# Kernel tuning notes

Measured on AMD Instinct MI355X. Metric: run time of the kernel, lower is better.

## Reference

```python
import jax, jax.numpy as jnp
import numpy as np

MARGIN = 1.0

def setup_inputs() -> dict:
    key = jax.random.key(0)
    k1, k2, k3 = jax.random.split(key, 3)
    B, C, D = 65536, 1000, 512
    x = jax.random.normal(k1, (B, D), dtype=jnp.float32)
    x = x / jnp.linalg.norm(x, axis=1, keepdims=True)  # docstring: ||x||2 = 1
    labels = jax.random.randint(k2, (B,), 0, C, dtype=jnp.int64)
    centers = jax.random.normal(k3, (C, D), dtype=jnp.float32)
    return {"x": x, "labels": labels, "centers": centers}

def reference(x, labels, centers):
    # l2Norm applied to the centers (module is only used when l2Norm is truthy)
    c = centers / jnp.linalg.norm(centers, axis=1, keepdims=True)  # (C, D)
    # cosine distance to every center: one batched GEMM instead of per-sample loop
    dist = 1.0 - jnp.einsum("bd,cd->bc", x, c)                      # (B, C)
    pos = jnp.take_along_axis(dist, labels[:, None], axis=1)[:, 0]  # (B,)
    # min over all classes != label: mask own class with +inf
    same = jnp.arange(c.shape[0])[None, :] == labels[:, None]       # (B, C)
    neg = jnp.min(jnp.where(same, jnp.inf, dist), axis=1)           # (B,)
    # sum of per-sample hinge losses divided by batch size == mean
    return jnp.mean(jax.nn.relu(pos + MARGIN - neg))
```

## Files before the change

kernel.cpp:

```cpp
#include <hip/hip_runtime.h>
#include <stdint.h>

typedef short v8s __attribute__((ext_vector_type(8)));
typedef short v4s __attribute__((ext_vector_type(4)));
typedef float v4f __attribute__((ext_vector_type(4)));

#define BM 256
#define BN 128
#define BKH 32
#define TSH ((BM + BN) * BKH)
#define POS_INF __builtin_inff()

typedef __attribute__((address_space(3))) unsigned int lds_uint;
typedef const __attribute__((address_space(1))) unsigned int glb_uint;

__device__ __forceinline__ void load16_lds(const void* g, void* l) {
    __builtin_amdgcn_global_load_lds((glb_uint*)g, (lds_uint*)l, 16, 0, 0);
}

__device__ __forceinline__ short f2bf(float f) {
    uint32_t u = __builtin_bit_cast(uint32_t, f);
    u += 0x7fffu + ((u >> 16) & 1u);
    return (short)(u >> 16);
}

__global__ void prep(const float* __restrict__ centers,
                     unsigned short* __restrict__ cbf,
                     int C, int D, int CP, int CB,
                     const float* __restrict__ x,
                     unsigned short* __restrict__ xbf, size_t nx,
                     int* __restrict__ cnt, int NB,
                     float* __restrict__ out) {
    const int b = blockIdx.x;
    const int t = threadIdx.x;
    if (b == 0 && t == 0) out[0] = 0.0f;
    if (b < CB) {
        const int g = b * 256 + t;
        if (g < NB) cnt[g] = 0;
        const int wave = t >> 6, lane = t & 63;
        const int row = b * 4 + wave;
        if (row >= CP) return;
        if (row >= C) {
            v4s z = {0, 0, 0, 0};
            for (int d = lane * 4; d < D; d += 256)
                *(v4s*)&cbf[(size_t)row * D + d] = z;
            return;
        }
        const float* src = centers + (size_t)row * D;
        float ss = 0.0f;
        for (int d = lane * 4; d < D; d += 256) {
            v4f f = *(const v4f*)&src[d];
            ss += f.x * f.x + f.y * f.y + f.z * f.z + f.w * f.w;
        }
        #pragma unroll
        for (int off = 32; off; off >>= 1) ss += __shfl_xor(ss, off, 64);
        const float rn = rsqrtf(ss);
        for (int d = lane * 4; d < D; d += 256) {
            v4f f = *(const v4f*)&src[d];
            v4s s;
            s.x = f2bf(f.x * rn); s.y = f2bf(f.y * rn);
            s.z = f2bf(f.z * rn); s.w = f2bf(f.w * rn);
            *(v4s*)&cbf[(size_t)row * D + d] = s;
        }
    } else {
        const size_t i = ((size_t)(b - CB) * 256 + t) * 8;
        if (i >= nx) return;
        v4f f0 = *(const v4f*)&x[i];
        v4f f1 = *(const v4f*)&x[i + 4];
        v8s s;
        s[0] = f2bf(f0.x); s[1] = f2bf(f0.y); s[2] = f2bf(f0.z); s[3] = f2bf(f0.w);
        s[4] = f2bf(f1.x); s[5] = f2bf(f1.y); s[6] = f2bf(f1.z); s[7] = f2bf(f1.w);
        *(v8s*)&xbf[i] = s;
    }
}

__global__ void __launch_bounds__(512)
gemm_fused(const unsigned short* __restrict__ xbf,
           const unsigned short* __restrict__ cbf,
           const int* __restrict__ labels,
           float* __restrict__ pos, float* __restrict__ partial,
           int* __restrict__ cnt,
           int Bt, int C, int D, int NT, float margin,
           float* __restrict__ out) {
    __shared__ short LDSbuf[2 * TSH];
    short* As0 = LDSbuf;
    short* Bs0 = LDSbuf + BM * BKH;
    short* As1 = LDSbuf + TSH;
    short* Bs1 = As1 + BM * BKH;

    const int t   = threadIdx.x;
    const int bid = blockIdx.x;
    const int xcd = bid & 7;
    const int per = bid >> 3;
    const int rowblk = (per >> 3) * 8 + xcd;
    const int nt     = per & 7;
    const int row0 = rowblk * BM;
    const int n0   = nt * BN;

    const int lane = t & 63;
    const int wave = t >> 6;
    const int wm = wave >> 1;
    const int wn = wave & 1;
    const int l15 = lane & 15, q = lane >> 4;

    const int rsub = lane >> 2;
    const int csrc = (lane & 3) ^ (rsub & 3);

    int myLab = 0;
    if (t < BM) myLab = labels[row0 + t];

    v4f acc[4][4];
    #pragma unroll
    for (int i = 0; i < 4; ++i)
        #pragma unroll
        for (int j = 0; j < 4; ++j)
            acc[i][j] = (v4f){0.f, 0.f, 0.f, 0.f};

    #define STAGE(As_, Bs_, k0_) do {                                        \
        load16_lds(&xbf[(size_t)(row0 + wave * 32 + rsub) * D + (k0_) + csrc * 8], \
                   &(As_)[(wave * 32) * BKH]);                               \
        load16_lds(&xbf[(size_t)(row0 + wave * 32 + 16 + rsub) * D + (k0_) + csrc * 8], \
                   &(As_)[(wave * 32 + 16) * BKH]);                          \
        load16_lds(&cbf[(size_t)(n0 + wave * 16 + rsub) * D + (k0_) + csrc * 8], \
                   &(Bs_)[(wave * 16) * BKH]);                               \
    } while (0)

    #define TILE(As_, Bs_) do {                                              \
        v8s a[4], b[4];                                                      \
        _Pragma("unroll")                                                    \
        for (int i = 0; i < 4; ++i)                                          \
            a[i] = *(const v8s*)&(As_)[(wm * 64 + i * 16 + l15) * BKH        \
                                       + ((q ^ (l15 & 3)) << 3)];            \
        _Pragma("unroll")                                                    \
        for (int j = 0; j < 4; ++j)                                          \
            b[j] = *(const v8s*)&(Bs_)[(wn * 64 + j * 16 + l15) * BKH        \
                                       + ((q ^ (l15 & 3)) << 3)];            \
        _Pragma("unroll")                                                    \
        for (int i = 0; i < 4; ++i)                                          \
            _Pragma("unroll")                                                \
            for (int j = 0; j < 4; ++j)                                      \
                acc[i][j] = __builtin_amdgcn_mfma_f32_16x16x32_bf16(         \
                    a[i], b[j], acc[i][j], 0, 0, 0);                         \
    } while (0)

    STAGE(As0, Bs0, 0);
    __syncthreads();

    const int KT2 = D / (2 * BKH);
    for (int kt2 = 0; kt2 < KT2; ++kt2) {
        const int k0 = kt2 * 64;
        STAGE(As1, Bs1, k0 + 32);
        TILE(As0, Bs0);
        __syncthreads();
        if (kt2 + 1 < KT2) STAGE(As0, Bs0, k0 + 64);
        TILE(As1, Bs1);
        __syncthreads();
    }

    #undef STAGE
    #undef TILE

    int*   Ls    = (int*)LDSbuf;
    float* sMinW = (float*)((char*)LDSbuf + 1024);
    int*   sLast = (int*)((char*)LDSbuf + 3072);
    float* wsum  = (float*)((char*)LDSbuf + 3088);
    if (t < BM) Ls[t] = myLab;
    __syncthreads();

    #pragma unroll
    for (int i = 0; i < 4; ++i) {
        #pragma unroll
        for (int rg = 0; rg < 4; ++rg) {
            const int row_l = wm * 64 + i * 16 + q * 4 + rg;
            const int lab = Ls[row_l];
            float m = POS_INF;
            #pragma unroll
            for (int j = 0; j < 4; ++j) {
                const int col = n0 + wn * 64 + j * 16 + l15;
                const float d = 1.0f - acc[i][j][rg];
                if (col == lab)
                    __hip_atomic_store(&pos[row0 + row_l], d,
                                       __ATOMIC_RELAXED, __HIP_MEMORY_SCOPE_AGENT);
                else if (col < C) m = fminf(m, d);
            }
            m = fminf(m, __shfl_xor(m, 1, 64));
            m = fminf(m, __shfl_xor(m, 2, 64));
            m = fminf(m, __shfl_xor(m, 4, 64));
            m = fminf(m, __shfl_xor(m, 8, 64));
            if (l15 == 0) sMinW[wn * BM + row_l] = m;
        }
    }
    __syncthreads();
    if (t < BM) {
        const float m = fminf(sMinW[t], sMinW[BM + t]);
        __hip_atomic_store(&partial[(size_t)nt * Bt + row0 + t], m,
                           __ATOMIC_RELAXED, __HIP_MEMORY_SCOPE_AGENT);
    }
    __syncthreads();

    if (t == 0) {
        __builtin_amdgcn_s_waitcnt(0);
        const int old = __hip_atomic_fetch_add(&cnt[rowblk], 1,
                                               __ATOMIC_RELAXED,
                                               __HIP_MEMORY_SCOPE_AGENT);
        *sLast = (old == NT - 1);
    }
    __syncthreads();
    if (!*sLast) return;

    float hng = 0.0f;
    if (t < BM) {
        const int r = row0 + t;
        float neg = POS_INF;
        for (int tt = 0; tt < NT; ++tt)
            neg = fminf(neg, __hip_atomic_load(&partial[(size_t)tt * Bt + r],
                                               __ATOMIC_RELAXED,
                                               __HIP_MEMORY_SCOPE_AGENT));
        const float p = __hip_atomic_load(&pos[r], __ATOMIC_RELAXED,
                                          __HIP_MEMORY_SCOPE_AGENT);
        hng = fmaxf(0.0f, p + margin - neg);
    }
    #pragma unroll
    for (int off = 32; off; off >>= 1) hng += __shfl_down(hng, off, 64);
    if (lane == 0) wsum[wave] = hng;
    __syncthreads();
    if (t == 0) {
        float s = 0.0f;
        #pragma unroll
        for (int w = 0; w < 8; ++w) s += wsum[w];
        atomicAdd(out, s * (1.0f / (float)Bt));
    }
}

extern "C" void kernel_launch(void* const* d_in, const int* in_sizes, int n_in,
                              void* d_out, int out_size, void* d_ws, size_t ws_size,
                              hipStream_t stream) {
    const float* x       = (const float*)d_in[0];
    const int*   labels  = (const int*)d_in[1];
    const float* centers = (const float*)d_in[2];
    float* out = (float*)d_out;

    const int Bt = in_sizes[1];
    const int D  = in_sizes[0] / Bt;
    const int C  = in_sizes[2] / D;
    const int NT = (C + BN - 1) / BN;
    const int CP = NT * BN;
    const int NB = Bt / BM;

    char* ws = (char*)d_ws;
    unsigned short* cbf = (unsigned short*)ws;
    size_t off = (size_t)CP * D * 2;
    off = (off + 255) & ~(size_t)255;
    float* pos = (float*)(ws + off);      off += (size_t)Bt * 4;
    float* partial = (float*)(ws + off);  off += (size_t)NT * Bt * 4;
    int* cnt = (int*)(ws + off);          off += (size_t)NB * 4;
    off = (off + 255) & ~(size_t)255;
    unsigned short* xbf = (unsigned short*)(ws + off);

    const size_t nx = (size_t)Bt * D;
    const int CB = CP / 4;
    const int XB = (int)((nx / 8 + 255) / 256);
    prep<<<CB + XB, 256, 0, stream>>>(centers, cbf, C, D, CP, CB, x, xbf, nx,
                                      cnt, NB, out);

    gemm_fused<<<NB * NT, 512, 0, stream>>>(xbf, cbf, labels, pos, partial, cnt,
                                            Bt, C, D, NT, 1.0f, out);
}
```

Baseline: 291.9 us.

## Triple-buffer LDS tiles with vmcnt waits and change swizzle pattern

Replaces the double-buffered K loop, which had two full __syncthreads per pair of tiles, with a three-stage ring buffer held in dynamic shared memory. Each iteration waits only until the oldest stage's async global-to-LDS loads have landed (vmcnt(3)) and then issues a raw barrier, so two tiles of loads can be in flight while MFMAs run. The XOR swizzle for the LDS layout also changes to use bits 1-2 of the row index, aimed at cutting bank conflicts. LDS use rises to about 72KB per block, which may limit occupancy, and the hand-placed waitcnt relies on exactly three loads per stage.

Result: faster. 285.0 us (-2.3%).

```diff
diff --git a/kernel.cpp b/kernel.cpp
--- a/kernel.cpp
+++ b/kernel.cpp
@@ -8,6 +8,7 @@
 #define BM 256
 #define BN 128
 #define BKH 32
+#define ASH (BM * BKH)
 #define TSH ((BM + BN) * BKH)
 #define POS_INF __builtin_inff()
 
@@ -82,11 +83,7 @@
            int* __restrict__ cnt,
            int Bt, int C, int D, int NT, float margin,
            float* __restrict__ out) {
-    __shared__ short LDSbuf[2 * TSH];
-    short* As0 = LDSbuf;
-    short* Bs0 = LDSbuf + BM * BKH;
-    short* As1 = LDSbuf + TSH;
-    short* Bs1 = As1 + BM * BKH;
+    extern __shared__ short LDS[];
 
     const int t   = threadIdx.x;
     const int bid = blockIdx.x;
@@ -104,7 +101,7 @@
     const int l15 = lane & 15, q = lane >> 4;
 
     const int rsub = lane >> 2;
-    const int csrc = (lane & 3) ^ (rsub & 3);
+    const int csrc = (lane & 3) ^ ((lane >> 3) & 3);
 
     int myLab = 0;
     if (t < BM) myLab = labels[row0 + t];
@@ -116,25 +113,30 @@
         for (int j = 0; j < 4; ++j)
             acc[i][j] = (v4f){0.f, 0.f, 0.f, 0.f};
 
-    #define STAGE(As_, Bs_, k0_) do {                                        \
+    #define WAITVM3() do { asm volatile("s_waitcnt vmcnt(3)" ::: "memory"); } while (0)
+    #define WAITVM0() do { asm volatile("s_waitcnt vmcnt(0)" ::: "memory"); } while (0)
+    #define BARRIER() do { __builtin_amdgcn_s_barrier(); \
+                           __builtin_amdgcn_sched_barrier(0); } while (0)
+
+    #define STAGE(buf_, k0_) do {                                            \
         load16_lds(&xbf[(size_t)(row0 + wave * 32 + rsub) * D + (k0_) + csrc * 8], \
-                   &(As_)[(wave * 32) * BKH]);                               \
+                   &LDS[(buf_) + (wave * 32) * BKH]);                        \
         load16_lds(&xbf[(size_t)(row0 + wave * 32 + 16 + rsub) * D + (k0_) + csrc * 8], \
-                   &(As_)[(wave * 32 + 16) * BKH]);                          \
+                   &LDS[(buf_) + (wave * 32 + 16) * BKH]);                   \
         load16_lds(&cbf[(size_t)(n0 + wave * 16 + rsub) * D + (k0_) + csrc * 8], \
-                   &(Bs_)[(wave * 16) * BKH]);                               \
+                   &LDS[(buf_) + ASH + (wave * 16) * BKH]);                  \
     } while (0)
 
-    #define TILE(As_, Bs_) do {                                              \
+    #define TILE(buf_) do {                                                  \
         v8s a[4], b[4];                                                      \
         _Pragma("unroll")                                                    \
         for (int i = 0; i < 4; ++i)                                          \
-            a[i] = *(const v8s*)&(As_)[(wm * 64 + i * 16 + l15) * BKH        \
-                                       + ((q ^ (l15 & 3)) << 3)];            \
+            a[i] = *(const v8s*)&LDS[(buf_) + (wm * 64 + i * 16 + l15) * BKH \
+                                     + ((q ^ ((l15 >> 1) & 3)) << 3)];       \
         _Pragma("unroll")                                                    \
         for (int j = 0; j < 4; ++j)                                          \
-            b[j] = *(const v8s*)&(Bs_)[(wn * 64 + j * 16 + l15) * BKH        \
-                                       + ((q ^ (l15 & 3)) << 3)];            \
+            b[j] = *(const v8s*)&LDS[(buf_) + ASH + (wn * 64 + j * 16 + l15) * BKH \
+                                     + ((q ^ ((l15 >> 1) & 3)) << 3)];       \
         _Pragma("unroll")                                                    \
         for (int i = 0; i < 4; ++i)                                          \
             _Pragma("unroll")                                                \
@@ -143,27 +145,38 @@
                     a[i], b[j], acc[i][j], 0, 0, 0);                         \
     } while (0)
 
-    STAGE(As0, Bs0, 0);
-    __syncthreads();
-
-    const int KT2 = D / (2 * BKH);
-    for (int kt2 = 0; kt2 < KT2; ++kt2) {
-        const int k0 = kt2 * 64;
-        STAGE(As1, Bs1, k0 + 32);
-        TILE(As0, Bs0);
-        __syncthreads();
-        if (kt2 + 1 < KT2) STAGE(As0, Bs0, k0 + 64);
-        TILE(As1, Bs1);
-        __syncthreads();
-    }
+    int bc = 0, b1 = TSH, b2 = 2 * TSH;
+
+    STAGE(bc, 0);
+    STAGE(b1, BKH);
+
+    const int KT = D / BKH;
+    for (int kt = 0; kt + 2 < KT; ++kt) {
+        WAITVM3();
+        BARRIER();
+        STAGE(b2, (kt + 2) * BKH);
+        TILE(bc);
+        const int tmp = bc; bc = b1; b1 = b2; b2 = tmp;
+    }
+    WAITVM3();
+    BARRIER();
+    TILE(bc);
+    WAITVM0();
+    BARRIER();
+    TILE(b1);
 
     #undef STAGE
     #undef TILE
-
-    int*   Ls    = (int*)LDSbuf;
-    float* sMinW = (float*)((char*)LDSbuf + 1024);
-    int*   sLast = (int*)((char*)LDSbuf + 3072);
-    float* wsum  = (float*)((char*)LDSbuf + 3088);
+    #undef WAITVM3
+    #undef WAITVM0
+    #undef BARRIER
+
+    __syncthreads();
+
+    int*   Ls    = (int*)LDS;
+    float* sMinW = (float*)((char*)LDS + 1024);
+    int*   sLast = (int*)((char*)LDS + 3072);
+    float* wsum  = (float*)((char*)LDS + 3088);
     if (t < BM) Ls[t] = myLab;
     __syncthreads();
 
@@ -263,6 +276,13 @@
     prep<<<CB + XB, 256, 0, stream>>>(centers, cbf, C, D, CP, CB, x, xbf, nx,
                                       cnt, NB, out);
 
-    gemm_fused<<<NB * NT, 512, 0, stream>>>(xbf, cbf, labels, pos, partial, cnt,
-                                            Bt, C, D, NT, 1.0f, out);
-}
+    static bool lds_attr_set = false;
+    if (!lds_attr_set) {
+        hipFuncSetAttribute(reinterpret_cast<const void*>(gemm_fused),
+                            hipFuncAttributeMaxDynamicSharedMemorySize,
+                            3 * TSH * (int)sizeof(short));
+        lds_attr_set = true;
+    }
+    gemm_fused<<<NB * NT, 512, 3 * TSH * sizeof(short), stream>>>(
+        xbf, cbf, labels, pos, partial, cnt, Bt, C, D, NT, 1.0f, out);
+}
```
